# Kernel optimization log

Measured on AMD Instinct MI355X. Metric: run time of the kernel, lower is better.

## Reference

```python
import jax, jax.numpy as jnp
import numpy as np

EPS = 1e-5


def _bn(h, gamma, beta):
    # BatchNorm1d in training mode: batch statistics over node dim
    mu = h.mean(axis=0)
    var = h.var(axis=0)
    return gamma * (h - mu) * jax.lax.rsqrt(var + EPS) + beta


def _rgcn_layer(x, src, dst, etype, W, Wloop, b, n_dst):
    # Relation-specific gather-transform-scatter (DGL RelGraphConv, sum agg,
    # self-loop + bias, no regularizer).
    x_src = x[src]                                   # [E, in] gather
    num_rels = W.shape[0]
    m = jnp.zeros((x_src.shape[0], W.shape[2]), x.dtype)
    for r in range(num_rels):                        # small fixed relation count
        m = m + jnp.where((etype == r)[:, None], x_src @ W[r], 0.0)
    agg = jax.ops.segment_sum(m, dst, num_segments=n_dst)  # scatter-add to dst
    # DGL block convention: dst nodes are the prefix of src nodes
    return agg + x[:n_dst] @ Wloop + b


def setup_inputs() -> dict:
    key = jax.random.key(0)
    ks = jax.random.split(key, 16)
    N_SRC, N_DST0, N_DST1 = 200000, 50000, 10000
    E0, E1, R, H, C = 800000, 160000, 5, 256, 153
    s = 1.0 / np.sqrt(H)
    inp = {
        "x": jax.random.normal(ks[0], (N_SRC, H), jnp.float32),
        "src0": jax.random.randint(ks[1], (E0,), 0, N_SRC, jnp.int32),
        "dst0": jax.random.randint(ks[2], (E0,), 0, N_DST0, jnp.int32),
        "etype0": jax.random.randint(ks[3], (E0,), 0, R, jnp.int32),
        "src1": jax.random.randint(ks[4], (E1,), 0, N_DST0, jnp.int32),
        "dst1": jax.random.randint(ks[5], (E1,), 0, N_DST1, jnp.int32),
        "etype1": jax.random.randint(ks[6], (E1,), 0, R, jnp.int32),
        "n_dst0": N_DST0,
        "n_dst1": N_DST1,
        "W0": jax.random.normal(ks[7], (R, H, H), jnp.float32) * s,
        "Wl0": jax.random.normal(ks[8], (H, H), jnp.float32) * s,
        "b0": jnp.zeros((H,), jnp.float32),
        "g0": jnp.ones((H,), jnp.float32),
        "be0": jnp.zeros((H,), jnp.float32),
        "W1": jax.random.normal(ks[9], (R, H, H), jnp.float32) * s,
        "Wl1": jax.random.normal(ks[10], (H, H), jnp.float32) * s,
        "b1": jnp.zeros((H,), jnp.float32),
        "g1": jnp.ones((H,), jnp.float32),
        "be1": jnp.zeros((H,), jnp.float32),
        "Wm1": jax.random.normal(ks[11], (H, H), jnp.float32) * s,
        "bm1": jnp.zeros((H,), jnp.float32),
        "gm": jnp.ones((H,), jnp.float32),
        "bem": jnp.zeros((H,), jnp.float32),
        "Wm2": jax.random.normal(ks[12], (H, C), jnp.float32) * s,
        "bm2": jnp.zeros((C,), jnp.float32),
    }
    return inp


def reference(x, src0, dst0, etype0, src1, dst1, etype1, n_dst0, n_dst1,
              W0, Wl0, b0, g0, be0, W1, Wl1, b1, g1, be1,
              Wm1, bm1, gm, bem, Wm2, bm2):
    # layer 0
    h = _rgcn_layer(x, src0, dst0, etype0, W0, Wl0, b0, n_dst0)
    h = jax.nn.elu(_bn(h, g0, be0))
    # layer 1
    h = _rgcn_layer(h, src1, dst1, etype1, W1, Wl1, b1, n_dst1)
    h = jax.nn.elu(_bn(h, g1, be1))
    # MLP head (dropout is identity in eval)
    h = jax.nn.relu(_bn(h @ Wm1 + bm1, gm, bem))
    return h @ Wm2 + bm2
```

## Files before the change

### kernel.cpp

```cpp
#include <hip/hip_runtime.h>
#include <hip/hip_bf16.h>


#define HD   256
#define EPS  1e-5f
#define NREL 5
#define ND0  50000
#define ND1  10000
#define BK   64
#define PAD  8

typedef unsigned short ushort_t;
using f32x4  = __attribute__((ext_vector_type(4))) float;
using short8 = __attribute__((ext_vector_type(8))) short;

__device__ __forceinline__ ushort_t f2b(float f) {
    union { float f; unsigned u; } x; x.f = f;
    unsigned r = x.u + 0x7FFF + ((x.u >> 16) & 1);
    return (ushort_t)(r >> 16);
}
__device__ __forceinline__ float b2f(ushort_t h) {
    union { unsigned u; float f; } x; x.u = ((unsigned)h) << 16;
    return x.f;
}

struct WconvArgs {
    const float* src[14];
    ushort_t*    dst[14];
    int          N[14];
};
__global__ void wconv_all_kernel(WconvArgs a) {
    int mat = blockIdx.x >> 8;
    int id = (blockIdx.x & 255) * 256 + threadIdx.x;
    int n = id >> 8, k = id & 255;
    int N = a.N[mat];
    float v = (n < N) ? a.src[mat][(size_t)k * N + n] : 0.f;
    a.dst[mat][id] = f2b(v);
}

__global__ void xconv_kernel(const float* __restrict__ x, ushort_t* __restrict__ xb,
                             int n4) {
    int id = blockIdx.x * 256 + threadIdx.x;
    if (id >= n4) return;
    float4 v = ((const float4*)x)[id];
    ushort4 o; o.x = f2b(v.x); o.y = f2b(v.y); o.z = f2b(v.z); o.w = f2b(v.w);
    ((ushort4*)xb)[id] = o;
}

__global__ void count2_kernel(const int* __restrict__ d0, const int* __restrict__ e0, int E0,
                              const int* __restrict__ d1, const int* __restrict__ e1, int E1,
                              int* __restrict__ cnt, int* __restrict__ pos) {
    int e = blockIdx.x * 256 + threadIdx.x;
    if (e < E0) {
        pos[e] = atomicAdd(&cnt[e0[e] * ND0 + d0[e]], 1);
    } else if (e < E0 + E1) {
        int i = e - E0;
        pos[e] = atomicAdd(&cnt[NREL * ND0 + e1[i] * ND1 + d1[i]], 1);
    }
}

__global__ void scan_block_kernel(const int* __restrict__ in, int* __restrict__ out,
                                  int* __restrict__ bsum, int nb) {
    __shared__ int ts[256];
    int tid = threadIdx.x;
    int base = blockIdx.x * 1024 + tid * 4;
    int v0 = (base + 0 < nb) ? in[base + 0] : 0;
    int v1 = (base + 1 < nb) ? in[base + 1] : 0;
    int v2 = (base + 2 < nb) ? in[base + 2] : 0;
    int v3 = (base + 3 < nb) ? in[base + 3] : 0;
    int tsum = v0 + v1 + v2 + v3;
    ts[tid] = tsum;
    __syncthreads();
    for (int d = 1; d < 256; d <<= 1) {
        int t = (tid >= d) ? ts[tid - d] : 0;
        __syncthreads();
        ts[tid] += t;
        __syncthreads();
    }
    int excl = ts[tid] - tsum;
    if (base + 0 < nb) out[base + 0] = excl;
    if (base + 1 < nb) out[base + 1] = excl + v0;
    if (base + 2 < nb) out[base + 2] = excl + v0 + v1;
    if (base + 3 < nb) out[base + 3] = excl + v0 + v1 + v2;
    if (tid == 255 && bsum) bsum[blockIdx.x] = ts[255];
}

__global__ void scan_add_kernel(int* __restrict__ out, const int* __restrict__ bsum, int nb) {
    int i = blockIdx.x * 256 + threadIdx.x;
    if (i < nb) out[i] += bsum[i >> 10];
}

__global__ void fill2_kernel(const int* __restrict__ s0, const int* __restrict__ d0,
                             const int* __restrict__ e0, int E0,
                             const int* __restrict__ s1, const int* __restrict__ d1,
                             const int* __restrict__ e1, int E1,
                             const int* __restrict__ pos, const int* __restrict__ off,
                             int* __restrict__ ssrc) {
    int e = blockIdx.x * 256 + threadIdx.x;
    if (e < E0) {
        ssrc[off[e0[e] * ND0 + d0[e]] + pos[e]] = s0[e];
    } else if (e < E0 + E1) {
        int i = e - E0;
        ssrc[off[NREL * ND0 + e1[i] * ND1 + d1[i]] + pos[e]] = s1[i];
    }
}

__global__ void gather_kernel(const ushort_t* __restrict__ feat, const int* __restrict__ ssrc,
                              const int* __restrict__ cnt, const int* __restrict__ off,
                              int nbuckets, ushort_t* __restrict__ out,
                              const float* __restrict__ sc, const float* __restrict__ sh) {
    int wave = (blockIdx.x * 256 + threadIdx.x) >> 6;
    int lane = threadIdx.x & 63;
    if (wave >= nbuckets) return;
    int deg = cnt[wave], s = off[wave];
    float4 scv = {0, 0, 0, 0}, shv = {0, 0, 0, 0};
    if (sc) { scv = ((const float4*)sc)[lane]; shv = ((const float4*)sh)[lane]; }
    float a0 = 0, a1 = 0, a2 = 0, a3 = 0;
    if (sc) {
        for (int j = 0; j < deg; j++) {
            ushort4 v = ((const ushort4*)(feat + (size_t)ssrc[s + j] * HD))[lane];
            float f0 = fmaf(b2f(v.x), scv.x, shv.x);
            float f1 = fmaf(b2f(v.y), scv.y, shv.y);
            float f2 = fmaf(b2f(v.z), scv.z, shv.z);
            float f3 = fmaf(b2f(v.w), scv.w, shv.w);
            a0 += f0 > 0.f ? f0 : expm1f(f0);
            a1 += f1 > 0.f ? f1 : expm1f(f1);
            a2 += f2 > 0.f ? f2 : expm1f(f2);
            a3 += f3 > 0.f ? f3 : expm1f(f3);
        }
    } else {
        int j = 0;
        for (; j + 2 <= deg; j += 2) {
            int r0 = ssrc[s + j], r1 = ssrc[s + j + 1];
            ushort4 v0 = ((const ushort4*)(feat + (size_t)r0 * HD))[lane];
            ushort4 v1 = ((const ushort4*)(feat + (size_t)r1 * HD))[lane];
            a0 += b2f(v0.x) + b2f(v1.x); a1 += b2f(v0.y) + b2f(v1.y);
            a2 += b2f(v0.z) + b2f(v1.z); a3 += b2f(v0.w) + b2f(v1.w);
        }
        if (j < deg) {
            ushort4 v = ((const ushort4*)(feat + (size_t)ssrc[s + j] * HD))[lane];
            a0 += b2f(v.x); a1 += b2f(v.y); a2 += b2f(v.z); a3 += b2f(v.w);
        }
    }
    ushort4 o; o.x = f2b(a0); o.y = f2b(a1); o.z = f2b(a2); o.w = f2b(a3);
    ((ushort4*)(out + (size_t)wave * HD))[lane] = o;
}

__global__ void bnprep_kernel(const float* __restrict__ sums, const float* __restrict__ g,
                              const float* __restrict__ be, float invM,
                              float* __restrict__ sc, float* __restrict__ sh) {
    int c = threadIdx.x;
    float mu = sums[c] * invM;
    float var = sums[HD + c] * invM - mu * mu;
    float s = g[c] * rsqrtf(var + EPS);
    sc[c] = s; sh[c] = be[c] - mu * s;
}

struct Seg {
    const ushort_t* A;
    const ushort_t* B;
    const float* sc;
    const float* sh;
    int act;
};
struct GemmArgs {
    Seg seg[6];
    int nseg;
    const float* bias;
    float* stats;
    ushort_t* Cb;
    float* Cf;
    int M, N;
};

template <int BM>
__launch_bounds__(256)
__global__ void gemm_mfma_kernel(GemmArgs g) {
    constexpr int F = BM / 32;
    __shared__ __align__(16) ushort_t As[BM][BK + PAD];
    __shared__ __align__(16) ushort_t Bs[BM][BK + PAD];
    int tid = threadIdx.x;
    int wave = tid >> 6, lane = tid & 63;
    int rq = lane >> 4, ci = lane & 15;
    int wm = (wave >> 1) * (BM / 2), wn = (wave & 1) * (BM / 2);
    int bm = blockIdx.y * BM, bn = blockIdx.x * BM;
    f32x4 acc[F][F] = {};
    int K = g.nseg * HD;

    for (int kk = 0; kk < K; kk += BK) {
        int si = kk >> 8;
        int kl = kk & 255;
        const ushort_t* Ap = g.seg[si].A;
        const ushort_t* Bp = g.seg[si].B;
        const float* sc = g.seg[si].sc;
#pragma unroll
        for (int it = 0; it < BM / 32; it++) {
            int idx = tid + it * 256;
            int row = idx >> 3, c8 = idx & 7;
            uint4 v = *(const uint4*)(Ap + (size_t)(bm + row) * HD + kl + c8 * 8);
            if (sc) {
                const float* sh = g.seg[si].sh;
                int act = g.seg[si].act;
                ushort_t* u = (ushort_t*)&v;
                int kb = kl + c8 * 8;
#pragma unroll
                for (int j = 0; j < 8; j++) {
                    float f = fmaf(b2f(u[j]), sc[kb + j], sh[kb + j]);
                    f = (act == 2) ? fmaxf(f, 0.f) : (f > 0.f ? f : expm1f(f));
                    u[j] = f2b(f);
                }
            }
            *(uint4*)&As[row][c8 * 8] = v;
        }
#pragma unroll
        for (int it = 0; it < BM / 32; it++) {
            int idx = tid + it * 256;
            int row = idx >> 3, c8 = idx & 7;
            *(uint4*)&Bs[row][c8 * 8] =
                *(const uint4*)(Bp + (size_t)(bn + row) * HD + kl + c8 * 8);
        }
        __syncthreads();
#pragma unroll
        for (int ks = 0; ks < BK; ks += 32) {
            int kq = ks + rq * 8;
            short8 a[F], b[F];
#pragma unroll
            for (int mi = 0; mi < F; mi++)
                a[mi] = *(const short8*)&As[wm + mi * 16 + ci][kq];
#pragma unroll
            for (int ni = 0; ni < F; ni++)
                b[ni] = *(const short8*)&Bs[wn + ni * 16 + ci][kq];
#pragma unroll
            for (int mi = 0; mi < F; mi++)
#pragma unroll
                for (int ni = 0; ni < F; ni++)
                    acc[mi][ni] = __builtin_amdgcn_mfma_f32_16x16x32_bf16(
                        a[mi], b[ni], acc[mi][ni], 0, 0, 0);
        }
        __syncthreads();
    }

#pragma unroll
    for (int ni = 0; ni < F; ni++) {
        int col = bn + wn + ni * 16 + ci;
        float bv = (col < g.N) ? g.bias[col] : 0.f;
#pragma unroll
        for (int mi = 0; mi < F; mi++)
#pragma unroll
            for (int reg = 0; reg < 4; reg++) acc[mi][ni][reg] += bv;
    }
    if (g.stats) {
#pragma unroll
        for (int ni = 0; ni < F; ni++) {
            float s = 0.f, s2 = 0.f;
#pragma unroll
            for (int mi = 0; mi < F; mi++)
#pragma unroll
                for (int reg = 0; reg < 4; reg++) {
                    int row = bm + wm + mi * 16 + rq * 4 + reg;
                    if (row < g.M) { float v = acc[mi][ni][reg]; s += v; s2 += v * v; }
                }
            s  += __shfl_xor(s, 16);  s  += __shfl_xor(s, 32);
            s2 += __shfl_xor(s2, 16); s2 += __shfl_xor(s2, 32);
            if (rq == 0) {
                int col = bn + wn + ni * 16 + ci;
                atomicAdd(&g.stats[col], s);
                atomicAdd(&g.stats[HD + col], s2);
            }
        }
    }
#pragma unroll
    for (int mi = 0; mi < F; mi++)
#pragma unroll
        for (int ni = 0; ni < F; ni++)
#pragma unroll
            for (int reg = 0; reg < 4; reg++) {
                int row = bm + wm + mi * 16 + rq * 4 + reg;
                int col = bn + wn + ni * 16 + ci;
                if (row < g.M && col < g.N) {
                    float v = acc[mi][ni][reg];
                    if (g.Cb) g.Cb[(size_t)row * HD + col] = f2b(v);
                    else      g.Cf[(size_t)row * g.N + col] = v;
                }
            }
}

extern "C" void kernel_launch(void* const* d_in, const int* in_sizes, int n_in,
                              void* d_out, int out_size, void* d_ws, size_t ws_size,
                              hipStream_t stream) {
    const float* x   = (const float*)d_in[0];
    const int* src0  = (const int*)d_in[1];
    const int* dst0  = (const int*)d_in[2];
    const int* et0   = (const int*)d_in[3];
    const int* src1  = (const int*)d_in[4];
    const int* dst1  = (const int*)d_in[5];
    const int* et1   = (const int*)d_in[6];
    const float* W0  = (const float*)d_in[9];
    const float* Wl0 = (const float*)d_in[10];
    const float* b0  = (const float*)d_in[11];
    const float* g0  = (const float*)d_in[12];
    const float* be0 = (const float*)d_in[13];
    const float* W1  = (const float*)d_in[14];
    const float* Wl1 = (const float*)d_in[15];
    const float* b1  = (const float*)d_in[16];
    const float* g1  = (const float*)d_in[17];
    const float* be1 = (const float*)d_in[18];
    const float* Wm1 = (const float*)d_in[19];
    const float* bm1 = (const float*)d_in[20];
    const float* gm  = (const float*)d_in[21];
    const float* bem = (const float*)d_in[22];
    const float* Wm2 = (const float*)d_in[23];
    const float* bm2 = (const float*)d_in[24];

    const int E0 = in_sizes[1];
    const int E1 = in_sizes[4];
    const int NOUT = in_sizes[24];
    const int NSRC = in_sizes[0] / HD;
    const int NBKT = NREL * ND0 + NREL * ND1;

    char* p = (char*)d_ws;
    ushort_t* Wt = (ushort_t*)p;  p += (size_t)14 * 65536 * 2;
    float* st    = (float*)p;     p += 1536 * 4;
    float* bnp   = (float*)p;     p += 6 * 256 * 4;
    int* cnt     = (int*)p;       p += (size_t)NBKT * 4;
    int* off     = (int*)p;       p += (size_t)NBKT * 4;
    int* bsum    = (int*)p;       p += 1024 * 4;
    int* pos     = (int*)p;       p += (size_t)(E0 + E1) * 4;
    int* ssrc    = (int*)p;       p += (size_t)(E0 + E1) * 4;
    ushort_t* xb  = (ushort_t*)p; p += (size_t)NSRC * HD * 2;
    ushort_t* S0  = (ushort_t*)p; p += (size_t)(NREL * ND0 + 128) * HD * 2;
    ushort_t* S1  = (ushort_t*)p; p += (size_t)(NREL * ND1 + 128) * HD * 2;
    ushort_t* h0b = (ushort_t*)p; p += (size_t)(ND0 + 128) * HD * 2;
    ushort_t* h1b = (ushort_t*)p; p += (size_t)(ND1 + 128) * HD * 2;
    ushort_t* mb  = (ushort_t*)p; p += (size_t)(ND1 + 128) * HD * 2;

    float* st0 = st, *st1 = st + 512, *stm = st + 1024;
    float* sc0 = bnp, *sh0 = bnp + 256, *sc1 = bnp + 512, *sh1 = bnp + 768;
    float* scm = bnp + 1024, *shm = bnp + 1280;

    ushort_t* W0t  = Wt;
    ushort_t* Wl0t = Wt + 5 * 65536;
    ushort_t* W1t  = Wt + 6 * 65536;
    ushort_t* Wl1t = Wt + 11 * 65536;
    ushort_t* Wm1t = Wt + 12 * 65536;
    ushort_t* Wm2t = Wt + 13 * 65536;

    {
        WconvArgs wa;
        for (int r = 0; r < NREL; r++) { wa.src[r] = W0 + (size_t)r * 65536; wa.dst[r] = W0t + (size_t)r * 65536; wa.N[r] = 256; }
        wa.src[5] = Wl0; wa.dst[5] = Wl0t; wa.N[5] = 256;
        for (int r = 0; r < NREL; r++) { wa.src[6 + r] = W1 + (size_t)r * 65536; wa.dst[6 + r] = W1t + (size_t)r * 65536; wa.N[6 + r] = 256; }
        wa.src[11] = Wl1; wa.dst[11] = Wl1t; wa.N[11] = 256;
        wa.src[12] = Wm1; wa.dst[12] = Wm1t; wa.N[12] = 256;
        wa.src[13] = Wm2; wa.dst[13] = Wm2t; wa.N[13] = NOUT;
        wconv_all_kernel<<<14 * 256, 256, 0, stream>>>(wa);
    }
    xconv_kernel<<<(NSRC * 64 + 255) / 256, 256, 0, stream>>>(x, xb, NSRC * 64);
    hipMemsetAsync(st, 0, 1536 * sizeof(float), stream);
    hipMemsetAsync(cnt, 0, (size_t)NBKT * sizeof(int), stream);

    int ET = E0 + E1;
    count2_kernel<<<(ET + 255) / 256, 256, 0, stream>>>(dst0, et0, E0, dst1, et1, E1, cnt, pos);
    int nsb = (NBKT + 1023) / 1024;
    scan_block_kernel<<<nsb, 256, 0, stream>>>(cnt, off, bsum, NBKT);
    scan_block_kernel<<<1, 256, 0, stream>>>(bsum, bsum, nullptr, nsb);
    scan_add_kernel<<<(NBKT + 255) / 256, 256, 0, stream>>>(off, bsum, NBKT);
    fill2_kernel<<<(ET + 255) / 256, 256, 0, stream>>>(src0, dst0, et0, E0, src1, dst1, et1, E1, pos, off, ssrc);

    gather_kernel<<<(NREL * ND0 * 64) / 256, 256, 0, stream>>>(
        xb, ssrc, cnt, off, NREL * ND0, S0, nullptr, nullptr);
    {
        GemmArgs ga = {};
        for (int s = 0; s < NREL; s++)
            ga.seg[s] = { S0 + (size_t)s * ND0 * HD, W0t + (size_t)s * 65536, nullptr, nullptr, 0 };
        ga.seg[5] = { xb, Wl0t, nullptr, nullptr, 0 };
        ga.nseg = 6; ga.bias = b0; ga.stats = st0;
        ga.Cb = h0b; ga.Cf = nullptr; ga.M = ND0; ga.N = HD;
        gemm_mfma_kernel<128><<<dim3(2, (ND0 + 127) / 128), 256, 0, stream>>>(ga);
    }
    bnprep_kernel<<<1, 256, 0, stream>>>(st0, g0, be0, 1.f / ND0, sc0, sh0);

    gather_kernel<<<(NREL * ND1 * 64) / 256, 256, 0, stream>>>(
        h0b, ssrc, cnt + NREL * ND0, off + NREL * ND0, NREL * ND1, S1, sc0, sh0);
    {
        GemmArgs ga = {};
        for (int s = 0; s < NREL; s++)
            ga.seg[s] = { S1 + (size_t)s * ND1 * HD, W1t + (size_t)s * 65536, nullptr, nullptr, 0 };
        ga.seg[5] = { h0b, Wl1t, sc0, sh0, 1 };
        ga.nseg = 6; ga.bias = b1; ga.stats = st1;
        ga.Cb = h1b; ga.Cf = nullptr; ga.M = ND1; ga.N = HD;
        gemm_mfma_kernel<64><<<dim3(4, (ND1 + 63) / 64), 256, 0, stream>>>(ga);
    }
    bnprep_kernel<<<1, 256, 0, stream>>>(st1, g1, be1, 1.f / ND1, sc1, sh1);

    {
        GemmArgs ga = {};
        ga.seg[0] = { h1b, Wm1t, sc1, sh1, 1 };
        ga.nseg = 1; ga.bias = bm1; ga.stats = stm;
        ga.Cb = mb; ga.Cf = nullptr; ga.M = ND1; ga.N = HD;
        gemm_mfma_kernel<64><<<dim3(4, (ND1 + 63) / 64), 256, 0, stream>>>(ga);
    }
    bnprep_kernel<<<1, 256, 0, stream>>>(stm, gm, bem, 1.f / ND1, scm, shm);
    {
        GemmArgs ga = {};
        ga.seg[0] = { mb, Wm2t, scm, shm, 2 };
        ga.nseg = 1; ga.bias = bm2; ga.stats = nullptr;
        ga.Cb = nullptr; ga.Cf = (float*)d_out; ga.M = ND1; ga.N = NOUT;
        gemm_mfma_kernel<64><<<dim3((NOUT + 63) / 64, (ND1 + 63) / 64), 256, 0, stream>>>(ga);
    }
}
```

Baseline: 817.2 us.

## Load GEMM tiles directly into LDS in MFMA fragment layout

Replaces the padded row-major shared-memory tiles with a fragment-ordered layout in which each 16x32 MFMA fragment is stored contiguously per lane. The B tile, and the A tile when it needs no fused normalisation, are loaded with global_load_lds so the data bypasses registers. Fragment reads from LDS become linear and conflict-free. Launch bounds now request 4 blocks per CU, which may limit registers and cause spills.

```diff
diff --git a/kernel.cpp b/kernel.cpp
--- a/kernel.cpp
+++ b/kernel.cpp
@@ -8,7 +8,6 @@
 #define ND0  50000
 #define ND1  10000
 #define BK   64
-#define PAD  8
 
 typedef unsigned short ushort_t;
 using f32x4  = __attribute__((ext_vector_type(4))) float;
@@ -23,6 +22,11 @@
     union { unsigned u; float f; } x; x.u = ((unsigned)h) << 16;
     return x.f;
 }
+
+#define GLOAD_LDS16(gp, lp)                                                     \
+    __builtin_amdgcn_global_load_lds(                                           \
+        (const __attribute__((address_space(1))) unsigned int*)(gp),            \
+        (__attribute__((address_space(3))) unsigned int*)(lp), 16, 0, 0)
 
 struct WconvArgs {
     const float* src[14];
@@ -174,11 +178,13 @@
 };
 
 template <int BM>
-__launch_bounds__(256)
+__launch_bounds__(256, 4)
 __global__ void gemm_mfma_kernel(GemmArgs g) {
-    constexpr int F = BM / 32;
-    __shared__ __align__(16) ushort_t As[BM][BK + PAD];
-    __shared__ __align__(16) ushort_t Bs[BM][BK + PAD];
+    constexpr int F   = BM / 32;
+    constexpr int NFT = BM / 16;
+    constexpr int IT  = NFT * 2 / 4;
+    __shared__ __align__(1024) ushort_t As[NFT * 2 * 512];
+    __shared__ __align__(1024) ushort_t Bs[NFT * 2 * 512];
     int tid = threadIdx.x;
     int wave = tid >> 6, lane = tid & 63;
     int rq = lane >> 4, ci = lane & 15;
@@ -193,43 +199,52 @@
         const ushort_t* Ap = g.seg[si].A;
         const ushort_t* Bp = g.seg[si].B;
         const float* sc = g.seg[si].sc;
-#pragma unroll
-        for (int it = 0; it < BM / 32; it++) {
-            int idx = tid + it * 256;
-            int row = idx >> 3, c8 = idx & 7;
-            uint4 v = *(const uint4*)(Ap + (size_t)(bm + row) * HD + kl + c8 * 8);
-            if (sc) {
-                const float* sh = g.seg[si].sh;
-                int act = g.seg[si].act;
+        if (!sc) {
+#pragma unroll
+            for (int it = 0; it < IT; it++) {
+                int f = it * 4 + wave;
+                int mt = f >> 1, kt = f & 1;
+                const ushort_t* ga = Ap + (size_t)(bm + mt * 16 + ci) * HD
+                                        + kl + kt * 32 + rq * 8;
+                GLOAD_LDS16(ga, &As[f * 512 + lane * 8]);
+            }
+        } else {
+            const float* sh = g.seg[si].sh;
+            int act = g.seg[si].act;
+#pragma unroll
+            for (int it = 0; it < IT; it++) {
+                int f = it * 4 + wave;
+                int mt = f >> 1, kt = f & 1;
+                int kb = kl + kt * 32 + rq * 8;
+                uint4 v = *(const uint4*)(Ap + (size_t)(bm + mt * 16 + ci) * HD + kb);
                 ushort_t* u = (ushort_t*)&v;
-                int kb = kl + c8 * 8;
 #pragma unroll
                 for (int j = 0; j < 8; j++) {
-                    float f = fmaf(b2f(u[j]), sc[kb + j], sh[kb + j]);
-                    f = (act == 2) ? fmaxf(f, 0.f) : (f > 0.f ? f : expm1f(f));
-                    u[j] = f2b(f);
+                    float fv = fmaf(b2f(u[j]), sc[kb + j], sh[kb + j]);
+                    fv = (act == 2) ? fmaxf(fv, 0.f) : (fv > 0.f ? fv : expm1f(fv));
+                    u[j] = f2b(fv);
                 }
+                *(uint4*)&As[f * 512 + lane * 8] = v;
             }
-            *(uint4*)&As[row][c8 * 8] = v;
-        }
-#pragma unroll
-        for (int it = 0; it < BM / 32; it++) {
-            int idx = tid + it * 256;
-            int row = idx >> 3, c8 = idx & 7;
-            *(uint4*)&Bs[row][c8 * 8] =
-                *(const uint4*)(Bp + (size_t)(bn + row) * HD + kl + c8 * 8);
+        }
+#pragma unroll
+        for (int it = 0; it < IT; it++) {
+            int f = it * 4 + wave;
+            int nt = f >> 1, kt = f & 1;
+            const ushort_t* gb = Bp + (size_t)(bn + nt * 16 + ci) * HD
+                                    + kl + kt * 32 + rq * 8;
+            GLOAD_LDS16(gb, &Bs[f * 512 + lane * 8]);
         }
         __syncthreads();
 #pragma unroll
-        for (int ks = 0; ks < BK; ks += 32) {
-            int kq = ks + rq * 8;
+        for (int ks = 0; ks < 2; ks++) {
             short8 a[F], b[F];
 #pragma unroll
             for (int mi = 0; mi < F; mi++)
-                a[mi] = *(const short8*)&As[wm + mi * 16 + ci][kq];
+                a[mi] = *(const short8*)&As[((wm / 16 + mi) * 2 + ks) * 512 + lane * 8];
 #pragma unroll
             for (int ni = 0; ni < F; ni++)
-                b[ni] = *(const short8*)&Bs[wn + ni * 16 + ci][kq];
+                b[ni] = *(const short8*)&Bs[((wn / 16 + ni) * 2 + ks) * 512 + lane * 8];
 #pragma unroll
             for (int mi = 0; mi < F; mi++)
 #pragma unroll
```

After: 755.9 us. 1.08x faster.
